# Kernel optimization log

Measured on AMD Instinct MI355X. Metric: run time of the kernel, lower is better.

Reference implementation:

```python
import jax, jax.numpy as jnp
import numpy as np

DIM = 1024; DEPTH = 6; HEADS = 16; DH = 64; NF = 16; VOCAB = 20000; B = 4; N = 1024
INNER = HEADS * DH
FF_INNER = int(DIM * 4 * 2 / 3)  # GEGLU inner dim = 2730


def _ln(x, g):
    # torch F.layer_norm with beta=0 buffer, eps=1e-5
    m = x.mean(-1, keepdims=True)
    v = ((x - m) ** 2).mean(-1, keepdims=True)
    return (x - m) / jnp.sqrt(v + 1e-5) * g


def _attn(x, ctx, mask, ln_g, Wq, Wkv, Wo):
    # faithful: LayerNorm applied to x (queries); context, if given, used raw for k/v
    xn = _ln(x, ln_g)
    kv_x = xn if ctx is None else ctx
    b, i, _ = x.shape
    j = kv_x.shape[1]
    q = (xn @ Wq).reshape(b, i, HEADS, DH) * (DH ** -0.5)
    k, v = jnp.split(kv_x @ Wkv, 2, axis=-1)
    k = k.reshape(b, j, HEADS, DH)
    v = v.reshape(b, j, HEADS, DH)
    sim = jnp.einsum('bihd,bjhd->bhij', q, k)
    sim = jnp.where(mask, sim, -jnp.finfo(sim.dtype).max)
    attn = jax.nn.softmax(sim, axis=-1)
    out = jnp.einsum('bhij,bjhd->bihd', attn, v).reshape(b, i, INNER)
    return out @ Wo


def _closs(a, b, ls):
    # CLIP-style ContrastiveLossWithTemperature
    an = a / jnp.linalg.norm(a, axis=-1, keepdims=True)
    bn = b / jnp.linalg.norm(b, axis=-1, keepdims=True)
    logits = jnp.exp(ls) * (an @ bn.T)
    lab = jnp.arange(a.shape[0])
    la = -jax.nn.log_softmax(logits, axis=-1)[lab, lab].mean()
    lb = -jax.nn.log_softmax(logits.T, axis=-1)[lab, lab].mean()
    return (la + lb) * 0.5


def setup_inputs() -> dict:
    key = jax.random.key(0)
    ks = jax.random.split(key, 16)
    rn = lambda k, s: jax.random.normal(k, s, jnp.float32) * 0.02
    return {
        'spliced_data': jax.random.normal(ks[0], (B, N), jnp.float32),
        'spliced_index': jax.random.randint(ks[1], (B, N), 0, VOCAB),
        'emb': rn(ks[2], (VOCAB, DIM)),
        'fusion_tokens': jax.random.normal(ks[3], (NF, DIM), jnp.float32),
        'return_tokens': jax.random.normal(ks[4], (2, DIM), jnp.float32),
        'ln1_g': jnp.ones((DEPTH, DIM), jnp.float32),
        'Wq': rn(ks[5], (DEPTH, DIM, INNER)),
        'Wkv': rn(ks[6], (DEPTH, DIM, 2 * INNER)),
        'Wo': rn(ks[7], (DEPTH, INNER, DIM)),
        'ln2_g': jnp.ones((DEPTH, DIM), jnp.float32),
        'Wff1': rn(ks[8], (DEPTH, DIM, 2 * FF_INNER)),
        'Wff2': rn(ks[9], (DEPTH, FF_INNER, DIM)),
        'norm_g': jnp.ones((DIM,), jnp.float32),
        'pool_ln_g': jnp.ones((DIM,), jnp.float32),
        'pWq': rn(ks[10], (DIM, INNER)),
        'pWkv': rn(ks[11], (DIM, 2 * INNER)),
        'pWo': rn(ks[12], (INNER, DIM)),
        'logit_scale_c': jnp.float32(np.log(1.0 / 0.07)),
        'logit_scale_f': jnp.float32(np.log(1.0 / 0.07)),
    }


def reference(spliced_data, spliced_index, emb, fusion_tokens, return_tokens,
              ln1_g, Wq, Wkv, Wo, ln2_g, Wff1, Wff2, norm_g,
              pool_ln_g, pWq, pWkv, pWo, logit_scale_c, logit_scale_f):
    b = spliced_data.shape[0]
    # BioZorroEncoder: value-weighted embedding lookup
    spliced_tokens = emb[spliced_index] * spliced_data[..., None]  # [b, N, DIM]
    tokens = jnp.concatenate(
        [spliced_tokens, jnp.broadcast_to(fusion_tokens, (b, NF, DIM))], axis=1)
    tt = jnp.concatenate([jnp.zeros((N,), jnp.int32), jnp.ones((NF,), jnp.int32)])
    # spliced attends spliced; fusion attends everything
    zmask = (tt[:, None] == tt[None, :]) | (tt[:, None] == 1)

    def body(t, p):
        l1, wq, wkv, wo, l2, w1, w2 = p
        t = _attn(t, None, zmask, l1, wq, wkv, wo) + t
        h = _ln(t, l2) @ w1
        xh, gate = jnp.split(h, 2, axis=-1)
        t = (jax.nn.gelu(gate, approximate=False) * xh) @ w2 + t
        return t, None

    tokens, _ = jax.lax.scan(body, tokens, (ln1_g, Wq, Wkv, Wo, ln2_g, Wff1, Wff2))
    tokens = _ln(tokens, norm_g)

    rtt = jnp.array([0, 1], jnp.int32)
    pm0 = rtt[:, None] == tt[None, :]
    # faithful to source operator precedence: (pm0 | rtt) == GLOBAL(2) -> all False
    pm = (pm0.astype(jnp.int32) | rtt[:, None]) == 2

    ret = jnp.broadcast_to(return_tokens, (b, 2, DIM))
    pooled = _attn(ret, tokens, pm, pool_ln_g, pWq, pWkv, pWo) + ret

    spliced = pooled[:, 0]
    fusion = pooled[:, 1]
    loss = _closs(spliced, spliced, logit_scale_c) + _closs(spliced, fusion, logit_scale_f)
    return loss
```

## Files before the change

kernel.cpp:

```cpp
#include <hip/hip_runtime.h>

typedef unsigned short u16;
typedef unsigned long long u64;
typedef __attribute__((ext_vector_type(8))) short short8;
typedef __attribute__((ext_vector_type(4))) float f32x4;

__device__ __forceinline__ u16 f2b(float f) {
  union { float f; unsigned u; } x; x.f = f;
  unsigned r = x.u + 0x7fffu + ((x.u >> 16) & 1u);
  return (u16)(r >> 16);
}
__device__ __forceinline__ float b2f(u16 h) {
  union { unsigned u; float f; } x; x.u = ((unsigned)h) << 16;
  return x.f;
}
__device__ __forceinline__ void gld16(const void* g, void* l) {
  __builtin_amdgcn_global_load_lds(
      (__attribute__((address_space(1))) const void*)g,
      (__attribute__((address_space(3))) void*)l, 16, 0, 0);
}

__global__ __launch_bounds__(256) void embed_k(
    const float* __restrict__ data, const int* __restrict__ idx,
    const float* __restrict__ emb, const float* __restrict__ fus,
    float* __restrict__ t) {
  int row = blockIdx.x;
  int b = row / 1040, n = row % 1040;
  int tid = threadIdx.x;
  const float4* src;
  float sc = 1.f;
  if (n < 1024) {
    int e = idx[b * 1024 + n];
    sc = data[b * 1024 + n];
    src = (const float4*)(emb + (long)e * 1024);
  } else {
    src = (const float4*)(fus + (long)(n - 1024) * 1024);
  }
  float4 v = src[tid];
  v.x *= sc; v.y *= sc; v.z *= sc; v.w *= sc;
  ((float4*)(t + (long)row * 1024))[tid] = v;
}

__global__ __launch_bounds__(256) void wtrans5_k(
    const float* __restrict__ sWq, const float* __restrict__ sWkv,
    const float* __restrict__ sWo, const float* __restrict__ sW1,
    const float* __restrict__ sW2,
    u16* __restrict__ dQkvT, u16* __restrict__ dWoT,
    u16* __restrict__ dF1T, u16* __restrict__ dF2T) {
  int id = blockIdx.x;
  const float* src; u16* dst; int K, N, Kpad, nx; float sc = 1.f; int perm = 0;
  if (id < 1024)       { src = sWq;  dst = dQkvT;             K = 1024; N = 1024; Kpad = 1024; nx = 32; sc = 0.125f; }
  else if (id < 3072)  { id -= 1024; src = sWkv; dst = dQkvT + 1024 * 1024; K = 1024; N = 2048; Kpad = 1024; nx = 64; }
  else if (id < 4096)  { id -= 3072; src = sWo;  dst = dWoT;  K = 1024; N = 1024; Kpad = 1024; nx = 32; }
  else if (id < 9600)  { id -= 4096; src = sW1;  dst = dF1T;  K = 1024; N = 5504; Kpad = 1024; nx = 172; perm = 1; }
  else                 { id -= 9600; src = sW2;  dst = dF2T;  K = 2730; N = 1024; Kpad = 2752; nx = 32; }
  int n0 = (id % nx) * 32, k0 = (id / nx) * 32;
  __shared__ float tile[32][33];
  int x = threadIdx.x & 31, y = threadIdx.x >> 5;
#pragma unroll
  for (int i = 0; i < 4; i++) {
    int k = k0 + y + i * 8, n = n0 + x;
    float val = 0.f;
    if (perm) {
      int p = n >> 5, sub = n & 31;
      int o = (sub < 16) ? (p * 16 + sub) : (2714 + p * 16 + sub);
      bool ok = (sub < 16) ? (o < 2730) : (o < 5460);
      val = (k < K && ok) ? src[(long)k * 5460 + o] : 0.f;
    } else {
      val = (k < K && n < N) ? src[(long)k * N + n] * sc : 0.f;
    }
    tile[y + i * 8][x] = val;
  }
  __syncthreads();
#pragma unroll
  for (int i = 0; i < 4; i++) {
    int n = n0 + y + i * 8, k = k0 + x;
    dst[(long)n * Kpad + k] = f2b(tile[x][y + i * 8]);
  }
}

__global__ __launch_bounds__(256) void ln_k(
    const float* __restrict__ t, const float* __restrict__ g,
    u16* __restrict__ xn) {
  int row = blockIdx.x, tid = threadIdx.x;
  int wave = tid >> 6, lane = tid & 63;
  float4 v = ((const float4*)(t + (long)row * 1024))[tid];
  float s = v.x + v.y + v.z + v.w;
#pragma unroll
  for (int o = 32; o > 0; o >>= 1) s += __shfl_xor(s, o, 64);
  __shared__ float r1[4], r2[4];
  if (lane == 0) r1[wave] = s;
  __syncthreads();
  float mean = (r1[0] + r1[1] + r1[2] + r1[3]) * (1.f / 1024.f);
  float dx = v.x - mean, dy = v.y - mean, dz = v.z - mean, dw = v.w - mean;
  float q = dx * dx + dy * dy + dz * dz + dw * dw;
#pragma unroll
  for (int o = 32; o > 0; o >>= 1) q += __shfl_xor(q, o, 64);
  if (lane == 0) r2[wave] = q;
  __syncthreads();
  float var = (r2[0] + r2[1] + r2[2] + r2[3]) * (1.f / 1024.f);
  float inv = rsqrtf(var + 1e-5f);
  float4 gv = ((const float4*)g)[tid];
  u64 pack = (u64)f2b(dx * inv * gv.x)
           | ((u64)f2b(dy * inv * gv.y) << 16)
           | ((u64)f2b(dz * inv * gv.z) << 32)
           | ((u64)f2b(dw * inv * gv.w) << 48);
  *(u64*)(xn + (long)row * 1024 + tid * 4) = pack;
}

__global__ __launch_bounds__(256) void lnred_k(
    float* __restrict__ t, const float* __restrict__ p0, const float* __restrict__ p1,
    const float* __restrict__ g, u16* __restrict__ xn) {
  int row = blockIdx.x, tid = threadIdx.x;
  int wave = tid >> 6, lane = tid & 63;
  long base = (long)row * 1024;
  float4 v = ((const float4*)(t + base))[tid];
  float4 a = ((const float4*)(p0 + base))[tid];
  float4 bq = ((const float4*)(p1 + base))[tid];
  v.x += a.x + bq.x; v.y += a.y + bq.y; v.z += a.z + bq.z; v.w += a.w + bq.w;
  ((float4*)(t + base))[tid] = v;
  float s = v.x + v.y + v.z + v.w;
#pragma unroll
  for (int o = 32; o > 0; o >>= 1) s += __shfl_xor(s, o, 64);
  __shared__ float r1[4], r2[4];
  if (lane == 0) r1[wave] = s;
  __syncthreads();
  float mean = (r1[0] + r1[1] + r1[2] + r1[3]) * (1.f / 1024.f);
  float dx = v.x - mean, dy = v.y - mean, dz = v.z - mean, dw = v.w - mean;
  float q = dx * dx + dy * dy + dz * dz + dw * dw;
#pragma unroll
  for (int o = 32; o > 0; o >>= 1) q += __shfl_xor(q, o, 64);
  if (lane == 0) r2[wave] = q;
  __syncthreads();
  float var = (r2[0] + r2[1] + r2[2] + r2[3]) * (1.f / 1024.f);
  float inv = rsqrtf(var + 1e-5f);
  float4 gv = ((const float4*)g)[tid];
  u64 pack = (u64)f2b(dx * inv * gv.x)
           | ((u64)f2b(dy * inv * gv.y) << 16)
           | ((u64)f2b(dz * inv * gv.z) << 32)
           | ((u64)f2b(dw * inv * gv.w) << 48);
  *(u64*)(xn + base + tid * 4) = pack;
}

__global__ __launch_bounds__(256) void redrow_k(
    float* __restrict__ t, const float* __restrict__ p0, const float* __restrict__ p1,
    float* __restrict__ rowm, float* __restrict__ rinv) {
  int row = blockIdx.x, tid = threadIdx.x;
  int wave = tid >> 6, lane = tid & 63;
  long base = (long)row * 1024;
  float4 v = ((const float4*)(t + base))[tid];
  float4 a = ((const float4*)(p0 + base))[tid];
  float4 bq = ((const float4*)(p1 + base))[tid];
  v.x += a.x + bq.x; v.y += a.y + bq.y; v.z += a.z + bq.z; v.w += a.w + bq.w;
  ((float4*)(t + base))[tid] = v;
  float s = v.x + v.y + v.z + v.w;
#pragma unroll
  for (int o = 32; o > 0; o >>= 1) s += __shfl_xor(s, o, 64);
  __shared__ float r1[4], r2[4];
  if (lane == 0) r1[wave] = s;
  __syncthreads();
  float mean = (r1[0] + r1[1] + r1[2] + r1[3]) * (1.f / 1024.f);
  float dx = v.x - mean, dy = v.y - mean, dz = v.z - mean, dw = v.w - mean;
  float q = dx * dx + dy * dy + dz * dz + dw * dw;
#pragma unroll
  for (int o = 32; o > 0; o >>= 1) q += __shfl_xor(q, o, 64);
  if (lane == 0) r2[wave] = q;
  __syncthreads();
  if (tid == 0) {
    float var = (r2[0] + r2[1] + r2[2] + r2[3]) * (1.f / 1024.f);
    rowm[row] = mean;
    rinv[row] = rsqrtf(var + 1e-5f);
  }
}

__global__ __launch_bounds__(256) void gemm_bt(
    const u16* __restrict__ A, int lda,
    const u16* __restrict__ Bt, int ldb,
    void* __restrict__ C, int ldc,
    int K, int mode, int gx, int ns, long pstride, u16* __restrict__ vt) {
  __shared__ u16 As[3][128 * 32];
  __shared__ u16 Bs[3][128 * 32];
  int tid = threadIdx.x;
  int wave = tid >> 6, lane = tid & 63;
  int col = lane & 15, grp = lane >> 4;
  int nwg = gridDim.x;
  int id = blockIdx.x;
  int q = nwg >> 3, r = nwg & 7;
  int xcd = id & 7, off = id >> 3;
  int wgid = (xcd < r ? xcd * (q + 1) : r * (q + 1) + (xcd - r) * q) + off;
  int tiles = nwg / ns;
  int ksp = wgid / tiles;
  int rem = wgid % tiles;
  int bm = rem % gx, bn = rem / gx;
  int nst = K >> 5;
  int k0 = ((nst * ksp) / ns) << 5;
  int k1 = ((nst * (ksp + 1)) / ns) << 5;
  int sr = wave * 16 + (lane >> 2);
  int sk = ((lane & 3) ^ ((lane >> 3) & 3)) * 8;
  const u16* aSrc = A + ((long)bm * 128 + sr) * lda + sk;
  const u16* bSrc = Bt + ((long)bn * 128 + sr) * ldb + sk;
  int wm = (wave >> 1) * 64, wn = (wave & 1) * 64;
  f32x4 acc[4][4] = {};

#define GSTAGE(buf, kt) do { \
    _Pragma("unroll") \
    for (int qq = 0; qq < 2; qq++) { \
      gld16(aSrc + (kt) + (long)qq * 64 * lda, &As[buf][wave * 512 + qq * 2048]); \
      gld16(bSrc + (kt) + (long)qq * 64 * ldb, &Bs[buf][wave * 512 + qq * 2048]); \
    } } while (0)

  GSTAGE(0, k0);
  if (k0 + 32 < k1) GSTAGE(1, k0 + 32);
  int cur = 0;
  int slot = (grp ^ ((col >> 1) & 3)) * 8;
  for (int kt = k0; kt < k1; kt += 32) {
    if (kt + 64 < k1) {
      int nb = cur + 2; if (nb >= 3) nb -= 3;
      GSTAGE(nb, kt + 64);
      asm volatile("s_waitcnt vmcnt(8)" ::: "memory");
    } else if (kt + 32 < k1) {
      asm volatile("s_waitcnt vmcnt(4)" ::: "memory");
    } else {
      asm volatile("s_waitcnt vmcnt(0)" ::: "memory");
    }
    __builtin_amdgcn_s_barrier();
    __builtin_amdgcn_sched_barrier(0);
    short8 af[4], bfv[4];
#pragma unroll
    for (int m = 0; m < 4; m++)
      af[m] = *(const short8*)&As[cur][(wm + m * 16 + col) * 32 + slot];
#pragma unroll
    for (int n = 0; n < 4; n++)
      bfv[n] = *(const short8*)&Bs[cur][(wn + n * 16 + col) * 32 + slot];
    __builtin_amdgcn_s_setprio(1);
#pragma unroll
    for (int m = 0; m < 4; m++)
#pragma unroll
      for (int n = 0; n < 4; n++)
        acc[m][n] = __builtin_amdgcn_mfma_f32_16x16x32_bf16(af[m], bfv[n], acc[m][n], 0, 0, 0);
    __builtin_amdgcn_s_setprio(0);
    __builtin_amdgcn_s_barrier();
    __builtin_amdgcn_sched_barrier(0);
    cur = (cur == 2) ? 0 : cur + 1;
  }
#undef GSTAGE
  long r0 = (long)bm * 128 + wm + grp * 4;
  int c0 = bn * 128 + wn + col;
  if (mode == 3) {
    u16* Ab = (u16*)C;
#pragma unroll
    for (int m = 0; m < 4; m++)
#pragma unroll
      for (int np = 0; np < 2; np++) {
        int ac = ((bn * 4 + (wn >> 5) + np) << 4) + col;
#pragma unroll
        for (int rr = 0; rr < 4; rr++) {
          float xh = acc[m][np * 2][rr];
          float gt = acc[m][np * 2 + 1][rr];
          float rv = 0.f;
          if (ac < 2730)
            rv = 0.5f * gt * (1.f + erff(gt * 0.70710678118f)) * xh;
          Ab[(r0 + m * 16 + rr) * ldc + ac] = f2b(rv);
        }
      }
  } else if (mode != 1) {
    u16* Cb = (u16*)C;
#pragma unroll
    for (int m = 0; m < 4; m++)
#pragma unroll
      for (int n = 0; n < 4; n++)
#pragma unroll
        for (int rr = 0; rr < 4; rr++)
          Cb[(r0 + m * 16 + rr) * ldc + c0 + n * 16] = f2b(acc[m][n][rr]);
    if (mode == 2 && bn >= 16) {
#pragma unroll
      for (int m = 0; m < 4; m++) {
        long row = r0 + m * 16;
        if (row < 4160) {
          int bidx = (int)(row / 1040);
          int j = (int)(row - (long)bidx * 1040);
#pragma unroll
          for (int n = 0; n < 4; n++) {
            int d = c0 + n * 16 - 2048;
            u64 pack = (u64)f2b(acc[m][n][0])
                     | ((u64)f2b(acc[m][n][1]) << 16)
                     | ((u64)f2b(acc[m][n][2]) << 32)
                     | ((u64)f2b(acc[m][n][3]) << 48);
            *(u64*)(vt + ((long)(bidx * 16 + (d >> 6)) * 64 + (d & 63)) * 1040 + j) = pack;
          }
        }
      }
    }
  } else {
    float* Cf = (float*)C + (long)ksp * pstride;
#pragma unroll
    for (int m = 0; m < 4; m++)
#pragma unroll
      for (int n = 0; n < 4; n++)
#pragma unroll
        for (int rr = 0; rr < 4; rr++)
          Cf[(r0 + m * 16 + rr) * ldc + c0 + n * 16] = acc[m][n][rr];
  }
}

__global__ __launch_bounds__(256) void attn_k(
    const u16* __restrict__ qkv, const u16* __restrict__ vt,
    u16* __restrict__ out) {
  int nwg = gridDim.x;
  int id = blockIdx.x;
  int q = nwg >> 3, r = nwg & 7;
  int xcd = id & 7, off = id >> 3;
  int wgid = (xcd < r ? xcd * (q + 1) : r * (q + 1) + (xcd - r) * q) + off;
  int bh = wgid / 17, it = wgid % 17;
  int b = bh >> 4, h = bh & 15;
  int tid = threadIdx.x, wave = tid >> 6, lane = tid & 63;
  int col = lane & 15, grp = lane >> 4;
  int i0 = it * 64;
  int jmax = (it == 16) ? 1040 : 1024;
  const u16* qb = qkv + (long)b * 1040 * 3072 + h * 64;
  const u16* kb = qkv + (long)b * 1040 * 3072 + 1024 + h * 64;
  const u16* vb = vt + (long)bh * 64 * 1040;
  __shared__ u16 Ks[2][64 * 64];
  __shared__ u16 Vs[2][64 * 64];
  __shared__ u16 Ps[4][16 * 64];

  int srow0 = wave * 8 + (lane >> 3);
  int gsw = ((lane & 7) ^ (srow0 & 7)) * 8;
#define ASTAGE(buf, j0s) do { \
    int jv = (j0s) + gsw; if (jv >= 1040) jv = 1032; \
    _Pragma("unroll") \
    for (int qq = 0; qq < 2; qq++) { \
      int rr = qq * 32 + srow0; \
      gld16(kb + (long)((j0s) + rr) * 3072 + gsw, &Ks[buf][qq * 2048 + wave * 512]); \
      gld16(vb + (long)rr * 1040 + jv, &Vs[buf][qq * 2048 + wave * 512]); \
    } } while (0)

  short8 aq[2];
  int qrow = i0 + wave * 16;
#pragma unroll
  for (int kf = 0; kf < 2; kf++)
    aq[kf] = *(const short8*)(qb + (long)(qrow + col) * 3072 + kf * 32 + grp * 8);

  short8 one8 = {};
  if (col == 0) {
#pragma unroll
    for (int i = 0; i < 8; i++) one8[i] = (short)0x3F80;
  }

  f32x4 oa[4] = {};
  f32x4 oa1 = {};

  ASTAGE(0, 0);
  int cur = 0;
  for (int j0 = 0; j0 < jmax; j0 += 64) {
    if (j0 + 64 < jmax) {
      ASTAGE(cur ^ 1, j0 + 64);
      asm volatile("s_waitcnt vmcnt(4)" ::: "memory");
    } else {
      asm volatile("s_waitcnt vmcnt(0)" ::: "memory");
    }
    __builtin_amdgcn_s_barrier();
    __builtin_amdgcn_sched_barrier(0);
    f32x4 s[4] = {};
#pragma unroll
    for (int kf = 0; kf < 2; kf++) {
      short8 bk[4];
#pragma unroll
      for (int n = 0; n < 4; n++) {
        int rk = n * 16 + col;
        bk[n] = *(const short8*)&Ks[cur][rk * 64 + ((kf * 32 + grp * 8) ^ ((rk & 7) << 3))];
      }
      __builtin_amdgcn_s_setprio(1);
#pragma unroll
      for (int n = 0; n < 4; n++)
        s[n] = __builtin_amdgcn_mfma_f32_16x16x32_bf16(aq[kf], bk[n], s[n], 0, 0, 0);
      __builtin_amdgcn_s_setprio(0);
    }
    if (j0 + 64 > jmax) {
      int lim = jmax - j0;
#pragma unroll
      for (int n = 0; n < 4; n++) {
        if (n * 16 + col >= lim) {
#pragma unroll
          for (int r2 = 0; r2 < 4; r2++) s[n][r2] = -1e30f;
        }
      }
    }
#pragma unroll
    for (int r2 = 0; r2 < 4; r2++) {
      int rp = grp * 4 + r2;
#pragma unroll
      for (int n = 0; n < 4; n++) {
        float p = __expf(s[n][r2]);
        Ps[wave][rp * 64 + ((n * 16 + col) ^ ((rp & 7) << 3))] = f2b(p);
      }
    }
#pragma unroll
    for (int kf = 0; kf < 2; kf++) {
      short8 ap, bv[4];
      int rm = col;
      ap = *(const short8*)&Ps[wave][rm * 64 + ((kf * 32 + grp * 8) ^ ((rm & 7) << 3))];
#pragma unroll
      for (int n = 0; n < 4; n++) {
        int rv = n * 16 + col;
        bv[n] = *(const short8*)&Vs[cur][rv * 64 + ((kf * 32 + grp * 8) ^ ((rv & 7) << 3))];
      }
      __builtin_amdgcn_s_setprio(1);
#pragma unroll
      for (int n = 0; n < 4; n++)
        oa[n] = __builtin_amdgcn_mfma_f32_16x16x32_bf16(ap, bv[n], oa[n], 0, 0, 0);
      oa1 = __builtin_amdgcn_mfma_f32_16x16x32_bf16(ap, one8, oa1, 0, 0, 0);
      __builtin_amdgcn_s_setprio(0);
    }
    __builtin_amdgcn_s_barrier();
    __builtin_amdgcn_sched_barrier(0);
    cur ^= 1;
  }
#undef ASTAGE
  float lr[4];
#pragma unroll
  for (int r2 = 0; r2 < 4; r2++) lr[r2] = __shfl(oa1[r2], lane & 48, 64);
#pragma unroll
  for (int n = 0; n < 4; n++)
#pragma unroll
    for (int r2 = 0; r2 < 4; r2++) {
      int i = i0 + wave * 16 + grp * 4 + r2;
      if (i < 1040)
        out[((long)b * 1040 + i) * 1024 + h * 64 + n * 16 + col] = f2b(oa[n][r2] / lr[r2]);
    }
}

__global__ __launch_bounds__(256) void wcolsum_k(
    const float* __restrict__ t, const float* __restrict__ rowm,
    const float* __restrict__ rinv, float* __restrict__ colsum,
    float* __restrict__ msum) {
  int b = blockIdx.x, c = blockIdx.y, tid = threadIdx.x;
  float a0 = 0, a1 = 0, a2 = 0, a3 = 0, ms = 0;
  for (int r = 0; r < 20; r++) {
    long row = (long)b * 1040 + c * 20 + r;
    float iv = rinv[row];
    float4 v = ((const float4*)(t + row * 1024))[tid];
    a0 += v.x * iv; a1 += v.y * iv; a2 += v.z * iv; a3 += v.w * iv;
    if (tid == 0) ms += rowm[row] * iv;
  }
  atomicAdd(&colsum[b * 1024 + tid * 4 + 0], a0);
  atomicAdd(&colsum[b * 1024 + tid * 4 + 1], a1);
  atomicAdd(&colsum[b * 1024 + tid * 4 + 2], a2);
  atomicAdd(&colsum[b * 1024 + tid * 4 + 3], a3);
  if (tid == 0) atomicAdd(&msum[b], ms);
}

__global__ __launch_bounds__(256) void mv1_k(
    const float* __restrict__ colsum, const float* __restrict__ msum,
    const float* __restrict__ g, const float* __restrict__ pWkv,
    float* __restrict__ tmp) {
  int b = blockIdx.x, n = blockIdx.y * 256 + threadIdx.x;
  float msb = msum[b];
  float acc = 0.f;
  for (int k = 0; k < 1024; k++) {
    float mk = g[k] * (colsum[b * 1024 + k] - msb);
    acc += mk * pWkv[(long)k * 2048 + 1024 + n];
  }
  tmp[b * 1024 + n] = acc * (1.f / 1040.f);
}

__global__ __launch_bounds__(256) void mv2_k(
    const float* __restrict__ tmp, const float* __restrict__ pWo,
    const float* __restrict__ ret, float* __restrict__ spl,
    float* __restrict__ fub) {
  int b = blockIdx.x, n = blockIdx.y * 256 + threadIdx.x;
  float acc = 0.f;
  for (int k = 0; k < 1024; k++) acc += tmp[b * 1024 + k] * pWo[(long)k * 1024 + n];
  spl[b * 1024 + n] = ret[n] + acc;
  fub[b * 1024 + n] = ret[1024 + n] + acc;
}

__device__ float closs_dev(const float L[4][4]) {
  float la = 0.f, lb = 0.f;
  for (int i = 0; i < 4; i++) {
    float mx = fmaxf(fmaxf(L[i][0], L[i][1]), fmaxf(L[i][2], L[i][3]));
    float sm = expf(L[i][0] - mx) + expf(L[i][1] - mx) + expf(L[i][2] - mx) + expf(L[i][3] - mx);
    la += mx + logf(sm) - L[i][i];
  }
  for (int j = 0; j < 4; j++) {
    float mx = fmaxf(fmaxf(L[0][j], L[1][j]), fmaxf(L[2][j], L[3][j]));
    float sm = expf(L[0][j] - mx) + expf(L[1][j] - mx) + expf(L[2][j] - mx) + expf(L[3][j] - mx);
    lb += mx + logf(sm) - L[j][j];
  }
  return 0.125f * (la + lb);
}

__global__ __launch_bounds__(256) void loss_k(
    const float* __restrict__ s, const float* __restrict__ f,
    const float* __restrict__ lsc, const float* __restrict__ lsf,
    float* __restrict__ out) {
  __shared__ float dots[36];
  int tid = threadIdx.x, wave = tid >> 6, lane = tid & 63;
  for (int d = wave; d < 36; d += 4) {
    const float *a, *bb;
    if (d < 16) { a = s + (d >> 2) * 1024; bb = s + (d & 3) * 1024; }
    else if (d < 32) { int e = d - 16; a = s + (e >> 2) * 1024; bb = f + (e & 3) * 1024; }
    else { a = f + (d - 32) * 1024; bb = a; }
    float p = 0.f;
    for (int k = lane; k < 1024; k += 64) p += a[k] * bb[k];
#pragma unroll
    for (int o = 32; o > 0; o >>= 1) p += __shfl_xor(p, o, 64);
    if (lane == 0) dots[d] = p;
  }
  __syncthreads();
  if (tid == 0) {
    float nS[4], nF[4];
    for (int i = 0; i < 4; i++) { nS[i] = sqrtf(dots[i * 4 + i]); nF[i] = sqrtf(dots[32 + i]); }
    float e1 = expf(lsc[0]), e2 = expf(lsf[0]);
    float L1[4][4], L2[4][4];
    for (int i = 0; i < 4; i++)
      for (int j = 0; j < 4; j++) {
        L1[i][j] = e1 * dots[i * 4 + j] / (nS[i] * nS[j]);
        L2[i][j] = e2 * dots[16 + i * 4 + j] / (nS[i] * nF[j]);
      }
    out[0] = closs_dev(L1) + closs_dev(L2);
  }
}

extern "C" void kernel_launch(void* const* d_in, const int* in_sizes, int n_in,
                              void* d_out, int out_size, void* d_ws, size_t ws_size,
                              hipStream_t stream) {
  (void)in_sizes; (void)n_in; (void)out_size; (void)ws_size;
  const float* sdata = (const float*)d_in[0];
  const int*   sidx  = (const int*)d_in[1];
  const float* emb   = (const float*)d_in[2];
  const float* fus   = (const float*)d_in[3];
  const float* ret   = (const float*)d_in[4];
  const float* ln1g  = (const float*)d_in[5];
  const float* Wq    = (const float*)d_in[6];
  const float* Wkv   = (const float*)d_in[7];
  const float* Wo    = (const float*)d_in[8];
  const float* ln2g  = (const float*)d_in[9];
  const float* Wff1  = (const float*)d_in[10];
  const float* Wff2  = (const float*)d_in[11];
  const float* normg = (const float*)d_in[12];
  const float* pWkv  = (const float*)d_in[15];
  const float* pWo   = (const float*)d_in[16];
  const float* lsc   = (const float*)d_in[17];
  const float* lsf   = (const float*)d_in[18];

  char* ws = (char*)d_ws;
  float* t   = (float*)(ws + 0L);
  u16* xn    = (u16*)(ws + 17301504L);
  char* U    = ws + 25952256L;
  u16* qkv   = (u16*)(U);
  u16* vtb   = (u16*)(U + 26738688L);
  u16* aout  = (u16*)(U + 35270656L);
  u16* ab    = (u16*)(U + 35270656L);
  float* par0 = (float*)(U);
  float* par1 = (float*)(U + 17301504L);
  char* WT   = ws + 95698944L;
  u16* qkvT  = (u16*)(WT);
  u16* WoT   = (u16*)(WT + 6291456L);
  u16* f1T   = (u16*)(WT + 8388608L);
  u16* f2T   = (u16*)(WT + 19660800L);
  char* FIN  = ws + 120995840L;
  float* rowm   = (float*)(FIN);
  float* rinvp  = (float*)(FIN + 16640L);
  float* colsum = (float*)(FIN + 33280L);
  float* msum   = (float*)(FIN + 49664L);
  float* tmp    = (float*)(FIN + 49728L);
  float* spl    = (float*)(FIN + 66112L);
  float* fub    = (float*)(FIN + 82496L);
  const long PSTR = 4224L * 1024;

  embed_k<<<4160, 256, 0, stream>>>(sdata, sidx, emb, fus, t);

  for (int l = 0; l < 6; l++) {
    wtrans5_k<<<12352, 256, 0, stream>>>(
        Wq + (long)l * 1024 * 1024, Wkv + (long)l * 1024 * 2048,
        Wo + (long)l * 1024 * 1024, Wff1 + (long)l * 1024 * 5460,
        Wff2 + (long)l * 2730 * 1024, qkvT, WoT, f1T, f2T);

    if (l == 0)
      ln_k<<<4160, 256, 0, stream>>>(t, ln1g, xn);
    else
      lnred_k<<<4160, 256, 0, stream>>>(t, par0, par1, ln1g + l * 1024, xn);

    gemm_bt<<<33 * 24, 256, 0, stream>>>(xn, 1024, qkvT, 1024, qkv, 3072, 1024, 2, 33, 1, 0, vtb);
    attn_k<<<1088, 256, 0, stream>>>(qkv, vtb, aout);
    gemm_bt<<<33 * 8 * 2, 256, 0, stream>>>(aout, 1024, WoT, 1024, par0, 1024, 1024, 1, 33, 2, PSTR, vtb);
    lnred_k<<<4160, 256, 0, stream>>>(t, par0, par1, ln2g + l * 1024, xn);
    gemm_bt<<<33 * 43, 256, 0, stream>>>(xn, 1024, f1T, 1024, ab, 2752, 1024, 3, 33, 1, 0, vtb);
    gemm_bt<<<33 * 8 * 2, 256, 0, stream>>>(ab, 2752, f2T, 2752, par0, 1024, 2752, 1, 33, 2, PSTR, vtb);
  }

  redrow_k<<<4160, 256, 0, stream>>>(t, par0, par1, rowm, rinvp);
  hipMemsetAsync(colsum, 0, 16448, stream);
  wcolsum_k<<<dim3(4, 52), 256, 0, stream>>>(t, rowm, rinvp, colsum, msum);
  mv1_k<<<dim3(4, 4), 256, 0, stream>>>(colsum, msum, normg, pWkv, tmp);
  mv2_k<<<dim3(4, 4), 256, 0, stream>>>(tmp, pWo, ret, spl, fub);
  loss_k<<<1, 256, 0, stream>>>(spl, fub, lsc, lsf, (float*)d_out);
}
```

Measured before the change: 1.896 ms.

## Replace split-K partial GEMMs with 64-row tiles that accumulate residual in place

```diff
diff --git a/kernel.cpp b/kernel.cpp
--- a/kernel.cpp
+++ b/kernel.cpp
@@ -108,17 +108,11 @@
   *(u64*)(xn + (long)row * 1024 + tid * 4) = pack;
 }
 
-__global__ __launch_bounds__(256) void lnred_k(
-    float* __restrict__ t, const float* __restrict__ p0, const float* __restrict__ p1,
-    const float* __restrict__ g, u16* __restrict__ xn) {
+__global__ __launch_bounds__(256) void rowstats_k(
+    const float* __restrict__ t, float* __restrict__ rowm, float* __restrict__ rinv) {
   int row = blockIdx.x, tid = threadIdx.x;
   int wave = tid >> 6, lane = tid & 63;
-  long base = (long)row * 1024;
-  float4 v = ((const float4*)(t + base))[tid];
-  float4 a = ((const float4*)(p0 + base))[tid];
-  float4 bq = ((const float4*)(p1 + base))[tid];
-  v.x += a.x + bq.x; v.y += a.y + bq.y; v.z += a.z + bq.z; v.w += a.w + bq.w;
-  ((float4*)(t + base))[tid] = v;
+  float4 v = ((const float4*)(t + (long)row * 1024))[tid];
   float s = v.x + v.y + v.z + v.w;
 #pragma unroll
   for (int o = 32; o > 0; o >>= 1) s += __shfl_xor(s, o, 64);
@@ -132,40 +126,6 @@
   for (int o = 32; o > 0; o >>= 1) q += __shfl_xor(q, o, 64);
   if (lane == 0) r2[wave] = q;
   __syncthreads();
-  float var = (r2[0] + r2[1] + r2[2] + r2[3]) * (1.f / 1024.f);
-  float inv = rsqrtf(var + 1e-5f);
-  float4 gv = ((const float4*)g)[tid];
-  u64 pack = (u64)f2b(dx * inv * gv.x)
-           | ((u64)f2b(dy * inv * gv.y) << 16)
-           | ((u64)f2b(dz * inv * gv.z) << 32)
-           | ((u64)f2b(dw * inv * gv.w) << 48);
-  *(u64*)(xn + base + tid * 4) = pack;
-}
-
-__global__ __launch_bounds__(256) void redrow_k(
-    float* __restrict__ t, const float* __restrict__ p0, const float* __restrict__ p1,
-    float* __restrict__ rowm, float* __restrict__ rinv) {
-  int row = blockIdx.x, tid = threadIdx.x;
-  int wave = tid >> 6, lane = tid & 63;
-  long base = (long)row * 1024;
-  float4 v = ((const float4*)(t + base))[tid];
-  float4 a = ((const float4*)(p0 + base))[tid];
-  float4 bq = ((const float4*)(p1 + base))[tid];
-  v.x += a.x + bq.x; v.y += a.y + bq.y; v.z += a.z + bq.z; v.w += a.w + bq.w;
-  ((float4*)(t + base))[tid] = v;
-  float s = v.x + v.y + v.z + v.w;
-#pragma unroll
-  for (int o = 32; o > 0; o >>= 1) s += __shfl_xor(s, o, 64);
-  __shared__ float r1[4], r2[4];
-  if (lane == 0) r1[wave] = s;
-  __syncthreads();
-  float mean = (r1[0] + r1[1] + r1[2] + r1[3]) * (1.f / 1024.f);
-  float dx = v.x - mean, dy = v.y - mean, dz = v.z - mean, dw = v.w - mean;
-  float q = dx * dx + dy * dy + dz * dz + dw * dw;
-#pragma unroll
-  for (int o = 32; o > 0; o >>= 1) q += __shfl_xor(q, o, 64);
-  if (lane == 0) r2[wave] = q;
-  __syncthreads();
   if (tid == 0) {
     float var = (r2[0] + r2[1] + r2[2] + r2[3]) * (1.f / 1024.f);
     rowm[row] = mean;
@@ -177,7 +137,7 @@
     const u16* __restrict__ A, int lda,
     const u16* __restrict__ Bt, int ldb,
     void* __restrict__ C, int ldc,
-    int K, int mode, int gx, int ns, long pstride, u16* __restrict__ vt) {
+    int K, int mode, int gx, u16* __restrict__ vt) {
   __shared__ u16 As[3][128 * 32];
   __shared__ u16 Bs[3][128 * 32];
   int tid = threadIdx.x;
@@ -188,13 +148,7 @@
   int q = nwg >> 3, r = nwg & 7;
   int xcd = id & 7, off = id >> 3;
   int wgid = (xcd < r ? xcd * (q + 1) : r * (q + 1) + (xcd - r) * q) + off;
-  int tiles = nwg / ns;
-  int ksp = wgid / tiles;
-  int rem = wgid % tiles;
-  int bm = rem % gx, bn = rem / gx;
-  int nst = K >> 5;
-  int k0 = ((nst * ksp) / ns) << 5;
-  int k1 = ((nst * (ksp + 1)) / ns) << 5;
+  int bm = wgid % gx, bn = wgid / gx;
   int sr = wave * 16 + (lane >> 2);
   int sk = ((lane & 3) ^ ((lane >> 3) & 3)) * 8;
   const u16* aSrc = A + ((long)bm * 128 + sr) * lda + sk;
@@ -209,16 +163,16 @@
       gld16(bSrc + (kt) + (long)qq * 64 * ldb, &Bs[buf][wave * 512 + qq * 2048]); \
     } } while (0)
 
-  GSTAGE(0, k0);
-  if (k0 + 32 < k1) GSTAGE(1, k0 + 32);
+  GSTAGE(0, 0);
+  if (32 < K) GSTAGE(1, 32);
   int cur = 0;
   int slot = (grp ^ ((col >> 1) & 3)) * 8;
-  for (int kt = k0; kt < k1; kt += 32) {
-    if (kt + 64 < k1) {
+  for (int kt = 0; kt < K; kt += 32) {
+    if (kt + 64 < K) {
       int nb = cur + 2; if (nb >= 3) nb -= 3;
       GSTAGE(nb, kt + 64);
       asm volatile("s_waitcnt vmcnt(8)" ::: "memory");
-    } else if (kt + 32 < k1) {
+    } else if (kt + 32 < K) {
       asm volatile("s_waitcnt vmcnt(4)" ::: "memory");
     } else {
       asm volatile("s_waitcnt vmcnt(0)" ::: "memory");
@@ -263,7 +217,7 @@
           Ab[(r0 + m * 16 + rr) * ldc + ac] = f2b(rv);
         }
       }
-  } else if (mode != 1) {
+  } else {
     u16* Cb = (u16*)C;
 #pragma unroll
     for (int m = 0; m < 4; m++)
@@ -291,16 +245,86 @@
         }
       }
     }
-  } else {
-    float* Cf = (float*)C + (long)ksp * pstride;
-#pragma unroll
-    for (int m = 0; m < 4; m++)
+  }
+}
+
+__global__ __launch_bounds__(256) void gemm64_rmw(
+    const u16* __restrict__ A, int lda,
+    const u16* __restrict__ Bt, int ldb,
+    float* __restrict__ T, int K, int gx) {
+  __shared__ u16 As[3][64 * 32];
+  __shared__ u16 Bs[3][128 * 32];
+  int tid = threadIdx.x;
+  int wave = tid >> 6, lane = tid & 63;
+  int col = lane & 15, grp = lane >> 4;
+  int nwg = gridDim.x;
+  int id = blockIdx.x;
+  int q = nwg >> 3, r = nwg & 7;
+  int xcd = id & 7, off = id >> 3;
+  int wgid = (xcd < r ? xcd * (q + 1) : r * (q + 1) + (xcd - r) * q) + off;
+  int bm = wgid % gx, bn = wgid / gx;
+  int sr = wave * 16 + (lane >> 2);
+  int sk = ((lane & 3) ^ ((lane >> 3) & 3)) * 8;
+  const u16* aSrc = A + ((long)bm * 64 + sr) * lda + sk;
+  const u16* bSrc = Bt + ((long)bn * 128 + sr) * ldb + sk;
+  int wm = (wave >> 1) * 32, wn = (wave & 1) * 64;
+  f32x4 acc[2][4] = {};
+
+#define GSTAGE64(buf, kt) do { \
+    gld16(aSrc + (kt), &As[buf][wave * 512]); \
+    _Pragma("unroll") \
+    for (int qq = 0; qq < 2; qq++) \
+      gld16(bSrc + (kt) + (long)qq * 64 * ldb, &Bs[buf][qq * 2048 + wave * 512]); \
+    } while (0)
+
+  GSTAGE64(0, 0);
+  if (32 < K) GSTAGE64(1, 32);
+  int cur = 0;
+  int slot = (grp ^ ((col >> 1) & 3)) * 8;
+  for (int kt = 0; kt < K; kt += 32) {
+    if (kt + 64 < K) {
+      int nb = cur + 2; if (nb >= 3) nb -= 3;
+      GSTAGE64(nb, kt + 64);
+      asm volatile("s_waitcnt vmcnt(6)" ::: "memory");
+    } else if (kt + 32 < K) {
+      asm volatile("s_waitcnt vmcnt(3)" ::: "memory");
+    } else {
+      asm volatile("s_waitcnt vmcnt(0)" ::: "memory");
+    }
+    __builtin_amdgcn_s_barrier();
+    __builtin_amdgcn_sched_barrier(0);
+    short8 af[2], bfv[4];
+#pragma unroll
+    for (int m = 0; m < 2; m++)
+      af[m] = *(const short8*)&As[cur][(wm + m * 16 + col) * 32 + slot];
+#pragma unroll
+    for (int n = 0; n < 4; n++)
+      bfv[n] = *(const short8*)&Bs[cur][(wn + n * 16 + col) * 32 + slot];
+    __builtin_amdgcn_s_setprio(1);
+#pragma unroll
+    for (int m = 0; m < 2; m++)
 #pragma unroll
       for (int n = 0; n < 4; n++)
-#pragma unroll
-        for (int rr = 0; rr < 4; rr++)
-          Cf[(r0 + m * 16 + rr) * ldc + c0 + n * 16] = acc[m][n][rr];
-  }
+        acc[m][n] = __builtin_amdgcn_mfma_f32_16x16x32_bf16(af[m], bfv[n], acc[m][n], 0, 0, 0);
+    __builtin_amdgcn_s_setprio(0);
+    __builtin_amdgcn_s_barrier();
+    __builtin_amdgcn_sched_barrier(0);
+    cur = (cur == 2) ? 0 : cur + 1;
+  }
+#undef GSTAGE64
+  long r0 = (long)bm * 64 + wm + grp * 4;
+  int c0 = bn * 128 + wn + col;
+#pragma unroll
+  for (int m = 0; m < 2; m++)
+#pragma unroll
+    for (int rr = 0; rr < 4; rr++) {
+      long row = r0 + m * 16 + rr;
+      if (row < 4160) {
+#pragma unroll
+        for (int n = 0; n < 4; n++)
+          T[row * 1024 + c0 + n * 16] += acc[m][n][rr];
+      }
+    }
 }
 
 __global__ __launch_bounds__(256) void attn_k(
@@ -552,8 +576,6 @@
   u16* vtb   = (u16*)(U + 26738688L);
   u16* aout  = (u16*)(U + 35270656L);
   u16* ab    = (u16*)(U + 35270656L);
-  float* par0 = (float*)(U);
-  float* par1 = (float*)(U + 17301504L);
   char* WT   = ws + 95698944L;
   u16* qkvT  = (u16*)(WT);
   u16* WoT   = (u16*)(WT + 6291456L);
@@ -567,7 +589,6 @@
   float* tmp    = (float*)(FIN + 49728L);
   float* spl    = (float*)(FIN + 66112L);
   float* fub    = (float*)(FIN + 82496L);
-  const long PSTR = 4224L * 1024;
 
   embed_k<<<4160, 256, 0, stream>>>(sdata, sidx, emb, fus, t);
 
@@ -577,20 +598,16 @@
         Wo + (long)l * 1024 * 1024, Wff1 + (long)l * 1024 * 5460,
         Wff2 + (long)l * 2730 * 1024, qkvT, WoT, f1T, f2T);
 
-    if (l == 0)
-      ln_k<<<4160, 256, 0, stream>>>(t, ln1g, xn);
-    else
-      lnred_k<<<4160, 256, 0, stream>>>(t, par0, par1, ln1g + l * 1024, xn);
-
-    gemm_bt<<<33 * 24, 256, 0, stream>>>(xn, 1024, qkvT, 1024, qkv, 3072, 1024, 2, 33, 1, 0, vtb);
+    ln_k<<<4160, 256, 0, stream>>>(t, ln1g + l * 1024, xn);
+    gemm_bt<<<33 * 24, 256, 0, stream>>>(xn, 1024, qkvT, 1024, qkv, 3072, 1024, 2, 33, vtb);
     attn_k<<<1088, 256, 0, stream>>>(qkv, vtb, aout);
-    gemm_bt<<<33 * 8 * 2, 256, 0, stream>>>(aout, 1024, WoT, 1024, par0, 1024, 1024, 1, 33, 2, PSTR, vtb);
-    lnred_k<<<4160, 256, 0, stream>>>(t, par0, par1, ln2g + l * 1024, xn);
-    gemm_bt<<<33 * 43, 256, 0, stream>>>(xn, 1024, f1T, 1024, ab, 2752, 1024, 3, 33, 1, 0, vtb);
-    gemm_bt<<<33 * 8 * 2, 256, 0, stream>>>(ab, 2752, f2T, 2752, par0, 1024, 2752, 1, 33, 2, PSTR, vtb);
-  }
-
-  redrow_k<<<4160, 256, 0, stream>>>(t, par0, par1, rowm, rinvp);
+    gemm64_rmw<<<66 * 8, 256, 0, stream>>>(aout, 1024, WoT, 1024, t, 1024, 66);
+    ln_k<<<4160, 256, 0, stream>>>(t, ln2g + l * 1024, xn);
+    gemm_bt<<<33 * 43, 256, 0, stream>>>(xn, 1024, f1T, 1024, ab, 2752, 1024, 3, 33, vtb);
+    gemm64_rmw<<<66 * 8, 256, 0, stream>>>(ab, 2752, f2T, 2752, t, 2752, 66);
+  }
+
+  rowstats_k<<<4160, 256, 0, stream>>>(t, rowm, rinvp);
   hipMemsetAsync(colsum, 0, 16448, stream);
   wcolsum_k<<<dim3(4, 52), 256, 0, stream>>>(t, rowm, rinvp, colsum, msum);
   mv1_k<<<dim3(4, 4), 256, 0, stream>>>(colsum, msum, normg, pWkv, tmp);
```

Result: no change. 1.933 ms (+1.9%).
